# Kernel tuning notes

Measured on AMD Instinct MI355X. Metric: run time of the kernel, lower is better.

The kernel has to match this reference:

```python
import jax, jax.numpy as jnp
import numpy as np

T = 8192          # total prefill tokens (single sequence, cu_seqlens=[0,T])
H = 16            # local num heads (k == v heads)
D = 128           # head_k_dim == head_v_dim
K = 4             # causal conv kernel width
CHUNK = 64        # chunk size used by chunk_kda
EPS = 1e-6


def setup_inputs() -> dict:
    key = jax.random.key(0)
    ks = jax.random.split(key, 6)
    return {
        "mixed_qkv": jax.random.normal(ks[0], (T, 3 * H * D), dtype=jnp.float32),
        "forget_gate": jax.random.normal(ks[1], (T, H * D), dtype=jnp.float32),
        "beta": jax.random.normal(ks[2], (T, H), dtype=jnp.float32),
        "conv_weights": jax.random.normal(ks[3], (3 * H * D, K), dtype=jnp.float32) * 0.1,
        "dt_bias": jax.random.normal(ks[4], (H, D), dtype=jnp.float32),
        "alog": jax.random.normal(ks[5], (H,), dtype=jnp.float32),
    }


def _l2norm(x):
    return x * jax.lax.rsqrt(jnp.sum(x * x, axis=-1, keepdims=True) + EPS)


def _causal_conv1d(x, w):
    # x: [T, C], w: [C, K] depthwise causal conv + SiLU (causal_conv1d_fn)
    xpad = jnp.pad(x, ((K - 1, 0), (0, 0)))
    out = sum(xpad[j:j + T] * w[:, j] for j in range(K))
    return jax.nn.silu(out)


def _kda_forward(mixed_qkv, forget_gate, beta, conv_weights, dt_bias, alog):
    x = _causal_conv1d(mixed_qkv, conv_weights)               # [T, 3*H*D]
    q, k, v = jnp.split(x, [H * D, 2 * H * D], axis=-1)
    q = _l2norm(q.reshape(T, H, D)) * (D ** -0.5)             # scale = head_k_dim^-0.5
    k = _l2norm(k.reshape(T, H, D))
    v = v.reshape(T, H, D)
    # fused_kda_gate: g = -exp(A_log) * softplus(g_raw + dt_bias), per (head, dim)
    g = -jnp.exp(alog)[None, :, None] * jax.nn.softplus(
        forget_gate.reshape(T, H, D) + dt_bias[None])
    decay = jnp.exp(g)                                        # [T, H, D]
    b = jax.nn.sigmoid(beta)                                  # [T, H]

    def step(S, inp):
        # S: [H, Dk, Dv]
        q_t, k_t, v_t, d_t, b_t = inp
        S = S * d_t[:, :, None]                               # per-dim forget gate on key dim
        kmem = jnp.einsum('hk,hkv->hv', k_t, S)
        delta = b_t[:, None] * (v_t - kmem)                   # beta-scaled delta rule
        S = S + jnp.einsum('hk,hv->hkv', k_t, delta)
        o_t = jnp.einsum('hk,hkv->hv', q_t, S)
        return S, o_t

    @jax.checkpoint
    def chunk_fn(S, ch):
        return jax.lax.scan(step, S, ch)

    NC = T // CHUNK
    chunked = lambda a: a.reshape(NC, CHUNK, H, D)
    S0 = jnp.zeros((H, D, D), dtype=jnp.float32)
    _, o = jax.lax.scan(chunk_fn, S0,
                        (chunked(q), chunked(k), chunked(v), chunked(decay),
                         b.reshape(NC, CHUNK, H)))
    return o.reshape(T, H, D)


def reference(mixed_qkv, forget_gate, beta, conv_weights, dt_bias, alog):
    return _kda_forward(mixed_qkv, forget_gate, beta, conv_weights, dt_bias, alog)
```

## Files before the change

### kernel.cpp

```cpp
#include <hip/hip_runtime.h>
#include <math.h>

#define NH 16
#define HD 128
#define CH1 2048
#define CH3 6144
#define CK 64
#define NC 128
#define PCH 132
#define MP 68

#define QT_OFF  0u
#define KBT_OFF 16777216u
#define U0_OFF  33554432u
#define Z_OFF   50331648u
#define W_OFF   67108864u
#define ECG_OFF 75497472u
#define SLAB_OFF 75759616u

__global__ __launch_bounds__(512, 2)
void kda_chunk(const float* __restrict__ mixed, const float* __restrict__ fg,
               const float* __restrict__ beta, const float* __restrict__ cw,
               const float* __restrict__ dtb, const float* __restrict__ alog,
               float* __restrict__ qt_g, float* __restrict__ kbt_g,
               float* __restrict__ u0_g, float* __restrict__ z_g,
               float* __restrict__ w_g, float* __restrict__ ecg_g) {
  __shared__ float lds[35520];
  float* kL  = lds;
  float* qL  = lds + 8448;
  float* cgL = lds + 16896;
  float* ML  = lds + 25344;
  float* NT  = lds + 29696;
  float* GB  = lds + 34048;
  float* bL  = lds + 34816;
  float* nrm = lds + 34880;

  const int tid = threadIdx.x;
  const int bid = blockIdx.x;
  const int c = bid >> 4, h = bid & 15;
  const int t0 = c * CK;
  const float ea = __expf(alog[h]);

  {
    size_t wb = (size_t)bid * 4096;
#pragma unroll
    for (int i = 0; i < 8; ++i) w_g[wb + tid + 512 * i] = 0.f;
  }

  for (int it = 0; it < 16; ++it) {
    int cell = tid + (it << 9);
    int d = cell & 127, t = cell >> 7;
    float x = fg[(size_t)(t0 + t) * CH1 + h * HD + d] + dtb[h * HD + d];
    float sp = (x > 20.f) ? x : log1pf(__expf(x));
    cgL[t * PCH + d] = -ea * sp;
  }
  if (tid < 64) bL[tid] = 1.f / (1.f + __expf(-beta[(size_t)(t0 + tid) * NH + h]));
  __syncthreads();

  if (tid < 128) {
    float a = 0.f;
    for (int t = 0; t < 64; ++t) { a += cgL[t * PCH + tid]; cgL[t * PCH + tid] = a; }
    ecg_g[(size_t)bid * 128 + tid] = __expf(a);
  }

  for (int it = 0; it < 32; ++it) {
    int cell = tid + (it << 9);
    int d = cell & 127, sec = (cell >> 7) & 1, t = cell >> 8;
    int ch = sec * CH1 + h * HD + d;
    float4 w4 = ((const float4*)cw)[ch];
    int rbase = t0 + t - 3;
    float acc;
    if (rbase >= 0) {
      const float* mp = mixed + (size_t)rbase * CH3 + ch;
      acc = mp[0] * w4.x + mp[CH3] * w4.y + mp[2 * CH3] * w4.z + mp[3 * CH3] * w4.w;
    } else {
      acc = 0.f;
      if (rbase + 0 >= 0) acc += mixed[(size_t)(rbase + 0) * CH3 + ch] * w4.x;
      if (rbase + 1 >= 0) acc += mixed[(size_t)(rbase + 1) * CH3 + ch] * w4.y;
      if (rbase + 2 >= 0) acc += mixed[(size_t)(rbase + 2) * CH3 + ch] * w4.z;
      acc += mixed[(size_t)(rbase + 3) * CH3 + ch] * w4.w;
    }
    acc = acc / (1.f + __expf(-acc));
    float* dst = (sec == 0) ? qL : kL;
    dst[t * PCH + d] = acc;
  }
  __syncthreads();

  {
    int sec = tid >> 8, t = (tid >> 2) & 63, r = tid & 3;
    const float* src = (sec == 0) ? qL : kL;
    float s = 0.f;
#pragma unroll
    for (int i = 0; i < 8; ++i) {
      float4 v = *(const float4*)(src + t * PCH + r * 32 + i * 4);
      s += v.x * v.x + v.y * v.y + v.z * v.z + v.w * v.w;
    }
    nrm[tid] = s;
  }
  __syncthreads();
  if (tid < 128) {
    int sec = tid >> 6, t = tid & 63;
    float s = nrm[sec * 256 + t * 4] + nrm[sec * 256 + t * 4 + 1] +
              nrm[sec * 256 + t * 4 + 2] + nrm[sec * 256 + t * 4 + 3];
    float inv = rsqrtf(s + 1e-6f);
    if (sec == 0) inv *= 0.08838834764831845f;
    nrm[512 + tid] = inv;
  }
  __syncthreads();
  for (int it = 0; it < 8; ++it) {
    int f4 = tid + (it << 9);
    int sec = f4 >> 11, t = (f4 >> 5) & 63, d4 = f4 & 31;
    float* dst = (sec == 0) ? qL : kL;
    float inv = nrm[512 + sec * 64 + t];
    float4 v = *(float4*)(dst + t * PCH + d4 * 4);
    v.x *= inv; v.y *= inv; v.z *= inv; v.w *= inv;
    *(float4*)(dst + t * PCH + d4 * 4) = v;
  }
  __syncthreads();

  {
    int tW = tid >> 3, g = tid & 7;
    size_t qb = (size_t)bid * 8192 + g * 1024 + tW * 16;
    size_t kb = (size_t)bid * 8192;
#pragma unroll
    for (int i = 0; i < 4; ++i) {
      int d = g * 16 + 4 * i;
      float4 qv = *(const float4*)(qL + tW * PCH + d);
      float4 cg4 = *(const float4*)(cgL + tW * PCH + d);
      float4 o;
      o.x = qv.x * __expf(cg4.x); o.y = qv.y * __expf(cg4.y);
      o.z = qv.z * __expf(cg4.z); o.w = qv.w * __expf(cg4.w);
      *(float4*)(qt_g + qb + 4 * i) = o;
      float4 kv = *(const float4*)(kL + tW * PCH + d);
      float4 c63 = *(const float4*)(cgL + 63 * PCH + d);
      kbt_g[kb + (size_t)(d + 0) * 64 + tW] = kv.x * __expf(c63.x - cg4.x);
      kbt_g[kb + (size_t)(d + 1) * 64 + tW] = kv.y * __expf(c63.y - cg4.y);
      kbt_g[kb + (size_t)(d + 2) * 64 + tW] = kv.z * __expf(c63.z - cg4.z);
      kbt_g[kb + (size_t)(d + 3) * 64 + tW] = kv.w * __expf(c63.w - cg4.w);
    }
  }

  if (tid < 136) {
    int L = tid;
    int tt = (int)((sqrtf(8.f * L + 1.f) - 1.f) * 0.5f);
    while ((tt + 1) * (tt + 2) / 2 <= L) ++tt;
    while (tt * (tt + 1) / 2 > L) --tt;
    int ss = L - tt * (tt + 1) / 2;
    int ta = tt * 4, sa = ss * 4;
    float accA[16], accW[16];
#pragma unroll
    for (int i = 0; i < 16; ++i) { accA[i] = 0.f; accW[i] = 0.f; }
    for (int d = 0; d < 128; d += 4) {
      float kt[4][4], qt4[4][4], ct[4][4], ks4[4][4], cs4[4][4];
#pragma unroll
      for (int i = 0; i < 4; ++i) {
        *(float4*)kt[i]  = *(const float4*)(kL + (ta + i) * PCH + d);
        *(float4*)qt4[i] = *(const float4*)(qL + (ta + i) * PCH + d);
        *(float4*)ct[i]  = *(const float4*)(cgL + (ta + i) * PCH + d);
        *(float4*)ks4[i] = *(const float4*)(kL + (sa + i) * PCH + d);
        *(float4*)cs4[i] = *(const float4*)(cgL + (sa + i) * PCH + d);
      }
#pragma unroll
      for (int i = 0; i < 4; ++i)
#pragma unroll
        for (int j = 0; j < 4; ++j)
#pragma unroll
          for (int dd = 0; dd < 4; ++dd) {
            float diff = ct[i][dd] - cs4[j][dd];
            float e = __expf(fminf(diff, 0.f));
            float m = e * ks4[j][dd];
            accA[i * 4 + j] += kt[i][dd] * m;
            accW[i * 4 + j] += qt4[i][dd] * m;
          }
    }
    size_t wb = (size_t)bid * 4096;
#pragma unroll
    for (int i = 0; i < 4; ++i)
#pragma unroll
      for (int j = 0; j < 4; ++j) {
        int t = ta + i, s = sa + j;
        if (s < t) ML[t * MP + s] = bL[t] * accA[i * 4 + j];
        float wv = (s <= t) ? accW[i * 4 + j] : 0.f;
        w_g[wb + (size_t)(s >> 3) * 512 + t * 8 + (s & 7)] = wv;
      }
  }
  __syncthreads();

  for (int i = tid; i < 4352; i += 512) NT[i] = 0.f;
  __syncthreads();
  if (tid < 64) {
    int b4 = tid >> 4, j = tid & 15, bo = b4 * 16;
    NT[(bo + j) * MP + bo + j] = 1.f;
    for (int t = j + 1; t < 16; ++t) {
      float s = 0.f;
      for (int sx = j; sx < t; ++sx)
        s += ML[(bo + t) * MP + bo + sx] * NT[(bo + j) * MP + bo + sx];
      NT[(bo + j) * MP + bo + t] = -s;
    }
  }
  __syncthreads();
  for (int lev = 1; lev <= 3; ++lev) {
    int nb = 4 - lev;
    for (int idx = tid; idx < nb * 256; idx += 512) {
      int J = idx >> 8, I = J + lev;
      int i = (idx >> 4) & 15, j = idx & 15;
      float s = 0.f;
      for (int P = J; P < I; ++P)
#pragma unroll 4
        for (int p = 0; p < 16; ++p)
          s += ML[(16 * I + i) * MP + 16 * P + p] * NT[(16 * J + j) * MP + 16 * P + p];
      GB[J * 256 + i * 16 + j] = s;
    }
    __syncthreads();
    for (int idx = tid; idx < nb * 256; idx += 512) {
      int J = idx >> 8, I = J + lev;
      int i = (idx >> 4) & 15, j = idx & 15;
      float s = 0.f;
#pragma unroll 4
      for (int p = 0; p < 16; ++p)
        s += NT[(16 * I + p) * MP + 16 * I + i] * GB[J * 256 + p * 16 + j];
      NT[(16 * J + j) * MP + 16 * I + i] = -s;
    }
    __syncthreads();
  }

  {
    int tW = tid >> 3, g = tid & 7;
    float b = bL[tW];
#pragma unroll
    for (int i = 0; i < 4; ++i) {
      int d = g * 16 + 4 * i;
      float4 kv = *(const float4*)(kL + tW * PCH + d);
      float4 cg4 = *(const float4*)(cgL + tW * PCH + d);
      float4 r;
      r.x = b * kv.x * __expf(cg4.x); r.y = b * kv.y * __expf(cg4.y);
      r.z = b * kv.z * __expf(cg4.z); r.w = b * kv.w * __expf(cg4.w);
      *(float4*)(qL + tW * PCH + d) = r;
    }
  }
  __syncthreads();
  {
    int t4 = tid >> 5, c4 = tid & 31;
    float acc[4][4];
#pragma unroll
    for (int i = 0; i < 4; ++i)
#pragma unroll
      for (int j = 0; j < 4; ++j) acc[i][j] = 0.f;
    for (int s = 0; s < 64; ++s) {
      float nv[4], rv[4];
      *(float4*)nv = *(const float4*)(NT + s * MP + t4 * 4);
      *(float4*)rv = *(const float4*)(qL + s * PCH + c4 * 4);
#pragma unroll
      for (int i = 0; i < 4; ++i)
#pragma unroll
        for (int j = 0; j < 4; ++j) acc[i][j] += nv[i] * rv[j];
    }
    size_t zb = (size_t)bid * 8192 + (size_t)(c4 >> 2) * 1024 + (c4 & 3) * 4;
#pragma unroll
    for (int i = 0; i < 4; ++i) {
      float4 o; o.x = acc[i][0]; o.y = acc[i][1]; o.z = acc[i][2]; o.w = acc[i][3];
      *(float4*)(z_g + zb + (size_t)(t4 * 4 + i) * 16) = o;
    }
  }
  __syncthreads();

  for (int it = 0; it < 16; ++it) {
    int cell = tid + (it << 9);
    int d = cell & 127, t = cell >> 7;
    int ch = 2 * CH1 + h * HD + d;
    float4 w4 = ((const float4*)cw)[ch];
    int rbase = t0 + t - 3;
    float acc;
    if (rbase >= 0) {
      const float* mp = mixed + (size_t)rbase * CH3 + ch;
      acc = mp[0] * w4.x + mp[CH3] * w4.y + mp[2 * CH3] * w4.z + mp[3 * CH3] * w4.w;
    } else {
      acc = 0.f;
      if (rbase + 0 >= 0) acc += mixed[(size_t)(rbase + 0) * CH3 + ch] * w4.x;
      if (rbase + 1 >= 0) acc += mixed[(size_t)(rbase + 1) * CH3 + ch] * w4.y;
      if (rbase + 2 >= 0) acc += mixed[(size_t)(rbase + 2) * CH3 + ch] * w4.z;
      acc += mixed[(size_t)(rbase + 3) * CH3 + ch] * w4.w;
    }
    acc = acc / (1.f + __expf(-acc));
    qL[t * PCH + d] = bL[t] * acc;
  }
  __syncthreads();
  {
    int t4 = tid >> 5, c4 = tid & 31;
    float acc[4][4];
#pragma unroll
    for (int i = 0; i < 4; ++i)
#pragma unroll
      for (int j = 0; j < 4; ++j) acc[i][j] = 0.f;
    for (int s = 0; s < 64; ++s) {
      float nv[4], rv[4];
      *(float4*)nv = *(const float4*)(NT + s * MP + t4 * 4);
      *(float4*)rv = *(const float4*)(qL + s * PCH + c4 * 4);
#pragma unroll
      for (int i = 0; i < 4; ++i)
#pragma unroll
        for (int j = 0; j < 4; ++j) acc[i][j] += nv[i] * rv[j];
    }
#pragma unroll
    for (int i = 0; i < 4; ++i) {
      size_t ob = ((size_t)(t0 + t4 * 4 + i) * NH + h) * HD + c4 * 4;
      float4 o; o.x = acc[i][0]; o.y = acc[i][1]; o.z = acc[i][2]; o.w = acc[i][3];
      *(float4*)(u0_g + ob) = o;
    }
  }
}

__global__ __launch_bounds__(512, 2)
void kda_scan3(const float* __restrict__ qt_g, const float* __restrict__ kbt_g,
               const float* __restrict__ u0_g, const float* __restrict__ z_g,
               const float* __restrict__ w_g, const float* __restrict__ ecg_g,
               float* __restrict__ out, float* __restrict__ slabs) {
  __shared__ float Tp[4224], Op[4224];
  __shared__ float Sl[1024];
  __shared__ float Un[512];
  __shared__ float Ut[512];
  (void)slabs;
  const int tid = threadIdx.x;
  const int bid = blockIdx.x;
  const int h = bid & 15, vg = bid >> 4;
  for (int i = tid; i < 1024; i += 512) Sl[i] = 0.f;
  __syncthreads();
  const int gA = tid >> 6, tA = tid & 63;
  const int tB = tid >> 3, jB = tid & 7;
  const int kC = tid & 127, j2 = tid >> 7;
  for (int c = 0; c < NC; ++c) {
    const int ch = c * 16 + h;
    float z[16], q[16];
    {
      const float* zb = z_g + (size_t)ch * 8192 + gA * 1024 + tA * 16;
      const float* qb = qt_g + (size_t)ch * 8192 + gA * 1024 + tA * 16;
#pragma unroll
      for (int i = 0; i < 4; ++i) {
        *(float4*)(z + 4 * i) = *(const float4*)(zb + 4 * i);
        *(float4*)(q + 4 * i) = *(const float4*)(qb + 4 * i);
      }
    }
    float w8[8];
    {
      const float* wb = w_g + (size_t)ch * 4096 + gA * 512 + tA * 8;
      *(float4*)w8 = *(const float4*)(wb);
      *(float4*)(w8 + 4) = *(const float4*)(wb + 4);
    }
    float kv64[64];
    {
      const float* kb = kbt_g + (size_t)ch * 8192 + (size_t)kC * 64;
#pragma unroll
      for (int t4 = 0; t4 < 16; ++t4)
        *(float4*)(kv64 + 4 * t4) = *(const float4*)(kb + 4 * t4);
    }
    const float u0v = u0_g[((size_t)(c * 64 + tB) * NH + h) * HD + vg * 8 + jB];
    const float eC = ecg_g[(size_t)ch * 128 + kC];

    float Ta[8], Oa[8];
#pragma unroll
    for (int j = 0; j < 8; ++j) { Ta[j] = 0.f; Oa[j] = 0.f; }
    const float* Sg = Sl + gA * 128;
#pragma unroll
    for (int dd = 0; dd < 16; ++dd) {
      float s8[8];
      *(float4*)s8 = *(const float4*)(Sg + dd * 8);
      *(float4*)(s8 + 4) = *(const float4*)(Sg + dd * 8 + 4);
      float zz = z[dd], qq = q[dd];
#pragma unroll
      for (int j = 0; j < 8; ++j) { Ta[j] += zz * s8[j]; Oa[j] += qq * s8[j]; }
    }
#pragma unroll
    for (int j = 0; j < 8; ++j) {
      Tp[gA * 528 + j * 66 + tA] = Ta[j];
      Op[gA * 528 + j * 66 + tA] = Oa[j];
    }
    __syncthreads();

    float Osave;
    {
      float Ts = 0.f, Os = 0.f;
#pragma unroll
      for (int g = 0; g < 8; ++g) {
        Ts += Tp[g * 528 + jB * 66 + tB];
        Os += Op[g * 528 + jB * 66 + tB];
      }
      float U = u0v - Ts;
      Un[tB * 8 + jB] = U;
      Ut[jB * 64 + tB] = U;
      Osave = Os;
    }
    __syncthreads();

    {
      float Wa[8];
#pragma unroll
      for (int j = 0; j < 8; ++j) Wa[j] = 0.f;
#pragma unroll
      for (int sp = 0; sp < 8; ++sp) {
        const float* ur = Un + (gA * 8 + sp) * 8;
        float u8[8];
        *(float4*)u8 = *(const float4*)(ur);
        *(float4*)(u8 + 4) = *(const float4*)(ur + 4);
        float wv = w8[sp];
#pragma unroll
        for (int j = 0; j < 8; ++j) Wa[j] += wv * u8[j];
      }
#pragma unroll
      for (int j = 0; j < 8; ++j) Tp[gA * 528 + j * 66 + tA] = Wa[j];
    }
    __syncthreads();

    {
      float O2 = 0.f;
#pragma unroll
      for (int g = 0; g < 8; ++g) O2 += Tp[g * 528 + jB * 66 + tB];
      out[((size_t)(c * 64 + tB) * NH + h) * HD + vg * 8 + jB] = Osave + O2;
    }

    {
      float a0 = 0.f, a1 = 0.f;
      const float* u0r = Ut + (2 * j2) * 64;
      const float* u1r = Ut + (2 * j2 + 1) * 64;
#pragma unroll
      for (int t4 = 0; t4 < 16; ++t4) {
        float4 ua = *(const float4*)(u0r + 4 * t4);
        float4 ub = *(const float4*)(u1r + 4 * t4);
        a0 += kv64[4 * t4 + 0] * ua.x + kv64[4 * t4 + 1] * ua.y +
              kv64[4 * t4 + 2] * ua.z + kv64[4 * t4 + 3] * ua.w;
        a1 += kv64[4 * t4 + 0] * ub.x + kv64[4 * t4 + 1] * ub.y +
              kv64[4 * t4 + 2] * ub.z + kv64[4 * t4 + 3] * ub.w;
      }
      float* sp2 = Sl + kC * 8 + 2 * j2;
      float s0 = sp2[0], s1 = sp2[1];
      sp2[0] = eC * s0 + a0;
      sp2[1] = eC * s1 + a1;
    }
    __syncthreads();
  }
}

extern "C" void kernel_launch(void* const* d_in, const int* in_sizes, int n_in,
                              void* d_out, int out_size, void* d_ws, size_t ws_size,
                              hipStream_t stream) {
  const float* mixed = (const float*)d_in[0];
  const float* fg    = (const float*)d_in[1];
  const float* beta  = (const float*)d_in[2];
  const float* cw    = (const float*)d_in[3];
  const float* dtb   = (const float*)d_in[4];
  const float* alog  = (const float*)d_in[5];
  float* ws = (float*)d_ws;
  float* qt_g  = ws + QT_OFF;
  float* kbt_g = ws + KBT_OFF;
  float* u0_g  = ws + U0_OFF;
  float* z_g   = ws + Z_OFF;
  float* w_g   = ws + W_OFF;
  float* ecg_g = ws + ECG_OFF;
  float* slabs = ws + SLAB_OFF;

  hipLaunchKernelGGL(kda_chunk, dim3(NC * NH), dim3(512), 0, stream,
                     mixed, fg, beta, cw, dtb, alog,
                     qt_g, kbt_g, u0_g, z_g, w_g, ecg_g);
  hipLaunchKernelGGL(kda_scan3, dim3(256), dim3(512), 0, stream,
                     qt_g, kbt_g, u0_g, z_g, w_g, ecg_g, (float*)d_out, slabs);
  (void)in_sizes; (void)n_in; (void)out_size; (void)ws_size;
}
```

Before: 1.973 ms.

## Double-buffer z/q prefetch across chunks in the scan kernel

Restructures the sequential chunk scan so the z and q loads for the next chunk are issued during the current chunk, using two register buffers and a loop unrolled by two. Empty asm statements force the global loads to complete before the first barrier, which keeps their latency off the serial critical path. The shared-memory padding strides also change (66 to 68, and Ut rows padded to 68). The cost is higher register pressure (an extra 32 floats per thread) under launch bounds of 512 threads and 2 blocks, which may cause spills.

```diff
diff --git a/kernel.cpp b/kernel.cpp
--- a/kernel.cpp
+++ b/kernel.cpp
@@ -310,132 +310,148 @@
   }
 }
 
+#define PT 68
+#define PG 544
+
+#define LOADZQ(zd, qd, cc) do {                                               \
+    const float* zb_ = z_g + (size_t)((cc) * 16 + h) * 8192 + gA * 1024 + tA * 16; \
+    const float* qb_ = qt_g + (size_t)((cc) * 16 + h) * 8192 + gA * 1024 + tA * 16; \
+    _Pragma("unroll")                                                         \
+    for (int i_ = 0; i_ < 4; ++i_) {                                          \
+      *(float4*)((zd) + 4 * i_) = *(const float4*)(zb_ + 4 * i_);             \
+      *(float4*)((qd) + 4 * i_) = *(const float4*)(qb_ + 4 * i_);             \
+    } } while (0)
+
+#define SCAN_BODY(zc, qc, zn, qn, c) do {                                     \
+    const int ch_ = (c) * 16 + h;                                             \
+                          \
+    { const float* kb_ = kbt_g + (size_t)ch_ * 8192 + (size_t)kC * 64;        \
+      _Pragma("unroll")                                                       \
+      for (int t4_ = 0; t4_ < 16; ++t4_)                                      \
+        *(float4*)(kv + 4 * t4_) = *(const float4*)(kb_ + 4 * t4_); }         \
+    { const float* wb_ = w_g + (size_t)ch_ * 4096 + gA * 512 + tA * 8;        \
+      *(float4*)w8 = *(const float4*)wb_;                                     \
+      *(float4*)(w8 + 4) = *(const float4*)(wb_ + 4); }                       \
+    u0v = u0_g[((size_t)((c) * 64 + tB) * NH + h) * HD + vg * 8 + jB];        \
+    eC = ecg_g[(size_t)ch_ * 128 + kC];                                       \
+                  \
+    { const int cn_ = ((c) + 1 < NC) ? (c) + 1 : NC - 1;                      \
+      LOADZQ(zn, qn, cn_); }                                                  \
+              \
+    { float Ta[8], Oa[8];                                                     \
+      _Pragma("unroll")                                                       \
+      for (int j = 0; j < 8; ++j) { Ta[j] = 0.f; Oa[j] = 0.f; }               \
+      const float* Sg = Sl + gA * 128;                                        \
+      _Pragma("unroll")                                                       \
+      for (int dd = 0; dd < 16; ++dd) {                                       \
+        float s8[8];                                                          \
+        *(float4*)s8 = *(const float4*)(Sg + dd * 8);                         \
+        *(float4*)(s8 + 4) = *(const float4*)(Sg + dd * 8 + 4);               \
+        float zz = (zc)[dd], qq = (qc)[dd];                                   \
+        _Pragma("unroll")                                                     \
+        for (int j = 0; j < 8; ++j) { Ta[j] += zz * s8[j]; Oa[j] += qq * s8[j]; } \
+      }                                                                       \
+      _Pragma("unroll")                                                       \
+      for (int j = 0; j < 8; ++j) {                                           \
+        Tp[gA * PG + j * PT + tA] = Ta[j];                                    \
+        Op[gA * PG + j * PT + tA] = Oa[j];                                    \
+      } }                                                                     \
+     \
+     \
+     \
+    _Pragma("unroll")                                                         \
+    for (int i_ = 0; i_ < 64; ++i_) asm volatile("" :: "v"(kv[i_]));          \
+    _Pragma("unroll")                                                         \
+    for (int i_ = 0; i_ < 8; ++i_) asm volatile("" :: "v"(w8[i_]));           \
+    _Pragma("unroll")                                                         \
+    for (int i_ = 0; i_ < 16; ++i_) asm volatile("" :: "v"((zn)[i_]));        \
+    _Pragma("unroll")                                                         \
+    for (int i_ = 0; i_ < 16; ++i_) asm volatile("" :: "v"((qn)[i_]));        \
+    asm volatile("" :: "v"(u0v), "v"(eC));                                    \
+    __syncthreads();                                                          \
+                 \
+    float Osave_;                                                             \
+    { float Ts = 0.f, Os = 0.f;                                               \
+      _Pragma("unroll")                                                       \
+      for (int g = 0; g < 8; ++g) {                                           \
+        Ts += Tp[g * PG + jB * PT + tB];                                      \
+        Os += Op[g * PG + jB * PT + tB];                                      \
+      }                                                                       \
+      float U = u0v - Ts;                                                     \
+      Un[tB * 8 + jB] = U;                                                    \
+      Ut[jB * PT + tB] = U;                                                   \
+      Osave_ = Os; }                                                          \
+    __syncthreads();                                                          \
+                   \
+    { float Wa[8];                                                            \
+      _Pragma("unroll")                                                       \
+      for (int j = 0; j < 8; ++j) Wa[j] = 0.f;                                \
+      _Pragma("unroll")                                                       \
+      for (int sp = 0; sp < 8; ++sp) {                                        \
+        const float* ur = Un + (gA * 8 + sp) * 8;                             \
+        float u8[8];                                                          \
+        *(float4*)u8 = *(const float4*)(ur);                                  \
+        *(float4*)(u8 + 4) = *(const float4*)(ur + 4);                        \
+        float wv = w8[sp];                                                    \
+        _Pragma("unroll")                                                     \
+        for (int j = 0; j < 8; ++j) Wa[j] += wv * u8[j];                      \
+      }                                                                       \
+      _Pragma("unroll")                                                       \
+      for (int j = 0; j < 8; ++j) Tp[gA * PG + j * PT + tA] = Wa[j]; }        \
+    __syncthreads();                                                          \
+                                           \
+    { float O2 = 0.f;                                                         \
+      _Pragma("unroll")                                                       \
+      for (int g = 0; g < 8; ++g) O2 += Tp[g * PG + jB * PT + tB];            \
+      out[((size_t)((c) * 64 + tB) * NH + h) * HD + vg * 8 + jB] = Osave_ + O2; } \
+                                        \
+    { float a0 = 0.f, a1 = 0.f;                                               \
+      const float* u0r = Ut + (2 * j2) * PT;                                  \
+      const float* u1r = Ut + (2 * j2 + 1) * PT;                              \
+      _Pragma("unroll")                                                       \
+      for (int t4 = 0; t4 < 16; ++t4) {                                       \
+        float4 ua = *(const float4*)(u0r + 4 * t4);                           \
+        float4 ub = *(const float4*)(u1r + 4 * t4);                           \
+        a0 += kv[4 * t4 + 0] * ua.x + kv[4 * t4 + 1] * ua.y +                 \
+              kv[4 * t4 + 2] * ua.z + kv[4 * t4 + 3] * ua.w;                  \
+        a1 += kv[4 * t4 + 0] * ub.x + kv[4 * t4 + 1] * ub.y +                 \
+              kv[4 * t4 + 2] * ub.z + kv[4 * t4 + 3] * ub.w;                  \
+      }                                                                       \
+      float* sp2 = Sl + kC * 8 + 2 * j2;                                      \
+      float s0 = sp2[0], s1 = sp2[1];                                         \
+      sp2[0] = eC * s0 + a0;                                                  \
+      sp2[1] = eC * s1 + a1; }                                                \
+    __syncthreads();                                                          \
+  } while (0)
+
 __global__ __launch_bounds__(512, 2)
 void kda_scan3(const float* __restrict__ qt_g, const float* __restrict__ kbt_g,
                const float* __restrict__ u0_g, const float* __restrict__ z_g,
                const float* __restrict__ w_g, const float* __restrict__ ecg_g,
                float* __restrict__ out, float* __restrict__ slabs) {
-  __shared__ float Tp[4224], Op[4224];
+  __shared__ float Tp[4352], Op[4352];
   __shared__ float Sl[1024];
   __shared__ float Un[512];
-  __shared__ float Ut[512];
+  __shared__ float Ut[544];
   (void)slabs;
   const int tid = threadIdx.x;
   const int bid = blockIdx.x;
   const int h = bid & 15, vg = bid >> 4;
-  for (int i = tid; i < 1024; i += 512) Sl[i] = 0.f;
-  __syncthreads();
   const int gA = tid >> 6, tA = tid & 63;
   const int tB = tid >> 3, jB = tid & 7;
   const int kC = tid & 127, j2 = tid >> 7;
-  for (int c = 0; c < NC; ++c) {
-    const int ch = c * 16 + h;
-    float z[16], q[16];
-    {
-      const float* zb = z_g + (size_t)ch * 8192 + gA * 1024 + tA * 16;
-      const float* qb = qt_g + (size_t)ch * 8192 + gA * 1024 + tA * 16;
-#pragma unroll
-      for (int i = 0; i < 4; ++i) {
-        *(float4*)(z + 4 * i) = *(const float4*)(zb + 4 * i);
-        *(float4*)(q + 4 * i) = *(const float4*)(qb + 4 * i);
-      }
-    }
-    float w8[8];
-    {
-      const float* wb = w_g + (size_t)ch * 4096 + gA * 512 + tA * 8;
-      *(float4*)w8 = *(const float4*)(wb);
-      *(float4*)(w8 + 4) = *(const float4*)(wb + 4);
-    }
-    float kv64[64];
-    {
-      const float* kb = kbt_g + (size_t)ch * 8192 + (size_t)kC * 64;
-#pragma unroll
-      for (int t4 = 0; t4 < 16; ++t4)
-        *(float4*)(kv64 + 4 * t4) = *(const float4*)(kb + 4 * t4);
-    }
-    const float u0v = u0_g[((size_t)(c * 64 + tB) * NH + h) * HD + vg * 8 + jB];
-    const float eC = ecg_g[(size_t)ch * 128 + kC];
-
-    float Ta[8], Oa[8];
-#pragma unroll
-    for (int j = 0; j < 8; ++j) { Ta[j] = 0.f; Oa[j] = 0.f; }
-    const float* Sg = Sl + gA * 128;
-#pragma unroll
-    for (int dd = 0; dd < 16; ++dd) {
-      float s8[8];
-      *(float4*)s8 = *(const float4*)(Sg + dd * 8);
-      *(float4*)(s8 + 4) = *(const float4*)(Sg + dd * 8 + 4);
-      float zz = z[dd], qq = q[dd];
-#pragma unroll
-      for (int j = 0; j < 8; ++j) { Ta[j] += zz * s8[j]; Oa[j] += qq * s8[j]; }
-    }
-#pragma unroll
-    for (int j = 0; j < 8; ++j) {
-      Tp[gA * 528 + j * 66 + tA] = Ta[j];
-      Op[gA * 528 + j * 66 + tA] = Oa[j];
-    }
-    __syncthreads();
-
-    float Osave;
-    {
-      float Ts = 0.f, Os = 0.f;
-#pragma unroll
-      for (int g = 0; g < 8; ++g) {
-        Ts += Tp[g * 528 + jB * 66 + tB];
-        Os += Op[g * 528 + jB * 66 + tB];
-      }
-      float U = u0v - Ts;
-      Un[tB * 8 + jB] = U;
-      Ut[jB * 64 + tB] = U;
-      Osave = Os;
-    }
-    __syncthreads();
-
-    {
-      float Wa[8];
-#pragma unroll
-      for (int j = 0; j < 8; ++j) Wa[j] = 0.f;
-#pragma unroll
-      for (int sp = 0; sp < 8; ++sp) {
-        const float* ur = Un + (gA * 8 + sp) * 8;
-        float u8[8];
-        *(float4*)u8 = *(const float4*)(ur);
-        *(float4*)(u8 + 4) = *(const float4*)(ur + 4);
-        float wv = w8[sp];
-#pragma unroll
-        for (int j = 0; j < 8; ++j) Wa[j] += wv * u8[j];
-      }
-#pragma unroll
-      for (int j = 0; j < 8; ++j) Tp[gA * 528 + j * 66 + tA] = Wa[j];
-    }
-    __syncthreads();
-
-    {
-      float O2 = 0.f;
-#pragma unroll
-      for (int g = 0; g < 8; ++g) O2 += Tp[g * 528 + jB * 66 + tB];
-      out[((size_t)(c * 64 + tB) * NH + h) * HD + vg * 8 + jB] = Osave + O2;
-    }
-
-    {
-      float a0 = 0.f, a1 = 0.f;
-      const float* u0r = Ut + (2 * j2) * 64;
-      const float* u1r = Ut + (2 * j2 + 1) * 64;
-#pragma unroll
-      for (int t4 = 0; t4 < 16; ++t4) {
-        float4 ua = *(const float4*)(u0r + 4 * t4);
-        float4 ub = *(const float4*)(u1r + 4 * t4);
-        a0 += kv64[4 * t4 + 0] * ua.x + kv64[4 * t4 + 1] * ua.y +
-              kv64[4 * t4 + 2] * ua.z + kv64[4 * t4 + 3] * ua.w;
-        a1 += kv64[4 * t4 + 0] * ub.x + kv64[4 * t4 + 1] * ub.y +
-              kv64[4 * t4 + 2] * ub.z + kv64[4 * t4 + 3] * ub.w;
-      }
-      float* sp2 = Sl + kC * 8 + 2 * j2;
-      float s0 = sp2[0], s1 = sp2[1];
-      sp2[0] = eC * s0 + a0;
-      sp2[1] = eC * s1 + a1;
-    }
-    __syncthreads();
+
+  float zA[16], qA[16], zB[16], qB[16];
+  float kv[64], w8[8];
+  float u0v, eC;
+
+  LOADZQ(zA, qA, 0);
+  for (int i = tid; i < 1024; i += 512) Sl[i] = 0.f;
+  __syncthreads();
+
+  for (int c = 0; c < NC; c += 2) {
+    SCAN_BODY(zA, qA, zB, qB, c);
+    SCAN_BODY(zB, qB, zA, qA, c + 1);
   }
 }
 
```

Result: slower. 2.161 ms (+9.5%).

## Split scan across 4-wide value slices and specialize thread roles per phase

Applied to the files above, without the earlier changes.

The sequential chunk scan now partitions the value dimension into 32 groups of 4 columns instead of 16 groups of 8, doubling the grid to 512 blocks so more CUs run the latency-bound recurrence in parallel. Within a block, the lower half of threads handles the U reduction and the state update while the upper half handles the output reduction and store, with padded shared-memory strides. Each block still reloads full z, q, w and kbt tiles for every chunk, so redundant global traffic doubles. Launch bounds also rise to 4 blocks per CU.

```diff
diff --git a/kernel.cpp b/kernel.cpp
--- a/kernel.cpp
+++ b/kernel.cpp
@@ -310,24 +310,29 @@
   }
 }
 
-__global__ __launch_bounds__(512, 2)
+#define PT 68
+#define PG 272
+
+__global__ __launch_bounds__(512, 4)
 void kda_scan3(const float* __restrict__ qt_g, const float* __restrict__ kbt_g,
                const float* __restrict__ u0_g, const float* __restrict__ z_g,
                const float* __restrict__ w_g, const float* __restrict__ ecg_g,
                float* __restrict__ out, float* __restrict__ slabs) {
-  __shared__ float Tp[4224], Op[4224];
-  __shared__ float Sl[1024];
-  __shared__ float Un[512];
-  __shared__ float Ut[512];
+  __shared__ float Tp[2176], Op[2176];
+  __shared__ float Sl[512];
+  __shared__ float Un[256];
+  __shared__ float Ut[272];
   (void)slabs;
   const int tid = threadIdx.x;
   const int bid = blockIdx.x;
   const int h = bid & 15, vg = bid >> 4;
-  for (int i = tid; i < 1024; i += 512) Sl[i] = 0.f;
-  __syncthreads();
   const int gA = tid >> 6, tA = tid & 63;
-  const int tB = tid >> 3, jB = tid & 7;
-  const int kC = tid & 127, j2 = tid >> 7;
+  const int tB = (tid >> 2) & 63, jB = tid & 3;
+  const int kC = tid & 127, j2 = (tid >> 7) & 1;
+
+  for (int i = tid; i < 512; i += 512) Sl[i] = 0.f;
+  __syncthreads();
+
   for (int c = 0; c < NC; ++c) {
     const int ch = c * 16 + h;
     float z[16], q[16];
@@ -346,91 +351,88 @@
       *(float4*)w8 = *(const float4*)(wb);
       *(float4*)(w8 + 4) = *(const float4*)(wb + 4);
     }
-    float kv64[64];
+    const float u0v = u0_g[((size_t)(c * 64 + tB) * NH + h) * HD + vg * 4 + jB];
+    float kv[64], eC = 0.f;
+    if (tid < 256) {
+      const float* kb = kbt_g + (size_t)ch * 8192 + (size_t)kC * 64;
+#pragma unroll
+      for (int t4 = 0; t4 < 16; ++t4)
+        *(float4*)(kv + 4 * t4) = *(const float4*)(kb + 4 * t4);
+      eC = ecg_g[(size_t)ch * 128 + kC];
+    }
+
     {
-      const float* kb = kbt_g + (size_t)ch * 8192 + (size_t)kC * 64;
-#pragma unroll
-      for (int t4 = 0; t4 < 16; ++t4)
-        *(float4*)(kv64 + 4 * t4) = *(const float4*)(kb + 4 * t4);
-    }
-    const float u0v = u0_g[((size_t)(c * 64 + tB) * NH + h) * HD + vg * 8 + jB];
-    const float eC = ecg_g[(size_t)ch * 128 + kC];
-
-    float Ta[8], Oa[8];
-#pragma unroll
-    for (int j = 0; j < 8; ++j) { Ta[j] = 0.f; Oa[j] = 0.f; }
-    const float* Sg = Sl + gA * 128;
-#pragma unroll
-    for (int dd = 0; dd < 16; ++dd) {
-      float s8[8];
-      *(float4*)s8 = *(const float4*)(Sg + dd * 8);
-      *(float4*)(s8 + 4) = *(const float4*)(Sg + dd * 8 + 4);
-      float zz = z[dd], qq = q[dd];
-#pragma unroll
-      for (int j = 0; j < 8; ++j) { Ta[j] += zz * s8[j]; Oa[j] += qq * s8[j]; }
-    }
-#pragma unroll
-    for (int j = 0; j < 8; ++j) {
-      Tp[gA * 528 + j * 66 + tA] = Ta[j];
-      Op[gA * 528 + j * 66 + tA] = Oa[j];
-    }
-    __syncthreads();
-
-    float Osave;
+      float Ta[4], Oa[4];
+#pragma unroll
+      for (int j = 0; j < 4; ++j) { Ta[j] = 0.f; Oa[j] = 0.f; }
+#pragma unroll
+      for (int dd = 0; dd < 16; ++dd) {
+        float s4[4];
+        *(float4*)s4 = *(const float4*)(Sl + (gA * 16 + dd) * 4);
+        float zz = z[dd], qq = q[dd];
+#pragma unroll
+        for (int j = 0; j < 4; ++j) { Ta[j] += zz * s4[j]; Oa[j] += qq * s4[j]; }
+      }
+#pragma unroll
+      for (int j = 0; j < 4; ++j) {
+        Tp[gA * PG + j * PT + tA] = Ta[j];
+        Op[gA * PG + j * PT + tA] = Oa[j];
+      }
+    }
+    __syncthreads();
+
+    float Osave = 0.f;
+    if (tid < 256) {
+      float Ts = 0.f;
+#pragma unroll
+      for (int g = 0; g < 8; ++g) Ts += Tp[g * PG + jB * PT + tB];
+      float U = u0v - Ts;
+      Un[tB * 4 + jB] = U;
+      Ut[jB * PT + tB] = U;
+    } else {
+      float Os = 0.f;
+#pragma unroll
+      for (int g = 0; g < 8; ++g) Os += Op[g * PG + jB * PT + tB];
+      Osave = Os;
+    }
+    __syncthreads();
+
     {
-      float Ts = 0.f, Os = 0.f;
-#pragma unroll
-      for (int g = 0; g < 8; ++g) {
-        Ts += Tp[g * 528 + jB * 66 + tB];
-        Os += Op[g * 528 + jB * 66 + tB];
-      }
-      float U = u0v - Ts;
-      Un[tB * 8 + jB] = U;
-      Ut[jB * 64 + tB] = U;
-      Osave = Os;
-    }
-    __syncthreads();
-
-    {
-      float Wa[8];
-#pragma unroll
-      for (int j = 0; j < 8; ++j) Wa[j] = 0.f;
+      float Wa[4];
+#pragma unroll
+      for (int j = 0; j < 4; ++j) Wa[j] = 0.f;
 #pragma unroll
       for (int sp = 0; sp < 8; ++sp) {
-        const float* ur = Un + (gA * 8 + sp) * 8;
-        float u8[8];
-        *(float4*)u8 = *(const float4*)(ur);
-        *(float4*)(u8 + 4) = *(const float4*)(ur + 4);
+        float u4[4];
+        *(float4*)u4 = *(const float4*)(Un + (gA * 8 + sp) * 4);
         float wv = w8[sp];
 #pragma unroll
-        for (int j = 0; j < 8; ++j) Wa[j] += wv * u8[j];
-      }
-#pragma unroll
-      for (int j = 0; j < 8; ++j) Tp[gA * 528 + j * 66 + tA] = Wa[j];
-    }
-    __syncthreads();
-
-    {
+        for (int j = 0; j < 4; ++j) Wa[j] += wv * u4[j];
+      }
+#pragma unroll
+      for (int j = 0; j < 4; ++j) Tp[gA * PG + j * PT + tA] = Wa[j];
+    }
+    __syncthreads();
+
+    if (tid >= 256) {
       float O2 = 0.f;
 #pragma unroll
-      for (int g = 0; g < 8; ++g) O2 += Tp[g * 528 + jB * 66 + tB];
-      out[((size_t)(c * 64 + tB) * NH + h) * HD + vg * 8 + jB] = Osave + O2;
-    }
-
-    {
+      for (int g = 0; g < 8; ++g) O2 += Tp[g * PG + jB * PT + tB];
+      out[((size_t)(c * 64 + tB) * NH + h) * HD + vg * 4 + jB] = Osave + O2;
+    } else {
       float a0 = 0.f, a1 = 0.f;
-      const float* u0r = Ut + (2 * j2) * 64;
-      const float* u1r = Ut + (2 * j2 + 1) * 64;
+      const float* u0r = Ut + (2 * j2) * PT;
+      const float* u1r = Ut + (2 * j2 + 1) * PT;
 #pragma unroll
       for (int t4 = 0; t4 < 16; ++t4) {
         float4 ua = *(const float4*)(u0r + 4 * t4);
         float4 ub = *(const float4*)(u1r + 4 * t4);
-        a0 += kv64[4 * t4 + 0] * ua.x + kv64[4 * t4 + 1] * ua.y +
-              kv64[4 * t4 + 2] * ua.z + kv64[4 * t4 + 3] * ua.w;
-        a1 += kv64[4 * t4 + 0] * ub.x + kv64[4 * t4 + 1] * ub.y +
-              kv64[4 * t4 + 2] * ub.z + kv64[4 * t4 + 3] * ub.w;
-      }
-      float* sp2 = Sl + kC * 8 + 2 * j2;
+        a0 += kv[4 * t4 + 0] * ua.x + kv[4 * t4 + 1] * ua.y +
+              kv[4 * t4 + 2] * ua.z + kv[4 * t4 + 3] * ua.w;
+        a1 += kv[4 * t4 + 0] * ub.x + kv[4 * t4 + 1] * ub.y +
+              kv[4 * t4 + 2] * ub.z + kv[4 * t4 + 3] * ub.w;
+      }
+      float* sp2 = Sl + kC * 4 + 2 * j2;
       float s0 = sp2[0], s1 = sp2[1];
       sp2[0] = eC * s0 + a0;
       sp2[1] = eC * s1 + a1;
@@ -460,7 +462,7 @@
   hipLaunchKernelGGL(kda_chunk, dim3(NC * NH), dim3(512), 0, stream,
                      mixed, fg, beta, cw, dtb, alog,
                      qt_g, kbt_g, u0_g, z_g, w_g, ecg_g);
-  hipLaunchKernelGGL(kda_scan3, dim3(256), dim3(512), 0, stream,
+  hipLaunchKernelGGL(kda_scan3, dim3(512), dim3(512), 0, stream,
                      qt_g, kbt_g, u0_g, z_g, w_g, ecg_g, (float*)d_out, slabs);
   (void)in_sizes; (void)n_in; (void)out_size; (void)ws_size;
 }
```

Result: slower. 2.264 ms (+14.7%).

## Warp-specialize scan into state-update and output groups, split chunk-prep dot over D

Applied to the files above, without the earlier changes.

The sequential scan kernel now splits its 512 threads into two halves. One half computes U and the state update, the other computes the output correction and writes the previous chunk's output, which removes one block barrier per chunk and defers the output write to the next iteration. Shared-memory strides are padded to cut bank conflicts. In the chunk-prep kernel, the triangular 4x4-tile dot products are split across two threads over halves of the head dimension and combined through shared memory, doubling active threads. The cost is an extra barrier and partial-sum traffic in prep, plus higher register and shared-memory use in the scan.

```diff
diff --git a/kernel.cpp b/kernel.cpp
--- a/kernel.cpp
+++ b/kernel.cpp
@@ -140,25 +140,27 @@
     }
   }
 
-  if (tid < 136) {
-    int L = tid;
+  int taD = 0, saD = 0;
+  float accA[16], accW[16];
+  if (tid < 272) {
+    int L = tid >> 1, dh = tid & 1;
     int tt = (int)((sqrtf(8.f * L + 1.f) - 1.f) * 0.5f);
     while ((tt + 1) * (tt + 2) / 2 <= L) ++tt;
     while (tt * (tt + 1) / 2 > L) --tt;
     int ss = L - tt * (tt + 1) / 2;
-    int ta = tt * 4, sa = ss * 4;
-    float accA[16], accW[16];
+    taD = tt * 4; saD = ss * 4;
 #pragma unroll
     for (int i = 0; i < 16; ++i) { accA[i] = 0.f; accW[i] = 0.f; }
-    for (int d = 0; d < 128; d += 4) {
+    int d0 = dh << 6;
+    for (int d = d0; d < d0 + 64; d += 4) {
       float kt[4][4], qt4[4][4], ct[4][4], ks4[4][4], cs4[4][4];
 #pragma unroll
       for (int i = 0; i < 4; ++i) {
-        *(float4*)kt[i]  = *(const float4*)(kL + (ta + i) * PCH + d);
-        *(float4*)qt4[i] = *(const float4*)(qL + (ta + i) * PCH + d);
-        *(float4*)ct[i]  = *(const float4*)(cgL + (ta + i) * PCH + d);
-        *(float4*)ks4[i] = *(const float4*)(kL + (sa + i) * PCH + d);
-        *(float4*)cs4[i] = *(const float4*)(cgL + (sa + i) * PCH + d);
+        *(float4*)kt[i]  = *(const float4*)(kL + (taD + i) * PCH + d);
+        *(float4*)qt4[i] = *(const float4*)(qL + (taD + i) * PCH + d);
+        *(float4*)ct[i]  = *(const float4*)(cgL + (taD + i) * PCH + d);
+        *(float4*)ks4[i] = *(const float4*)(kL + (saD + i) * PCH + d);
+        *(float4*)cs4[i] = *(const float4*)(cgL + (saD + i) * PCH + d);
       }
 #pragma unroll
       for (int i = 0; i < 4; ++i)
@@ -173,12 +175,28 @@
             accW[i * 4 + j] += qt4[i][dd] * m;
           }
     }
+    if (dh) {
+#pragma unroll
+      for (int i = 0; i < 16; ++i) {
+        NT[L * 32 + i] = accA[i];
+        NT[L * 32 + 16 + i] = accW[i];
+      }
+    }
+  }
+  __syncthreads();
+  if (tid < 272 && !(tid & 1)) {
+    int L = tid >> 1;
+#pragma unroll
+    for (int i = 0; i < 16; ++i) {
+      accA[i] += NT[L * 32 + i];
+      accW[i] += NT[L * 32 + 16 + i];
+    }
     size_t wb = (size_t)bid * 4096;
 #pragma unroll
     for (int i = 0; i < 4; ++i)
 #pragma unroll
       for (int j = 0; j < 4; ++j) {
-        int t = ta + i, s = sa + j;
+        int t = taD + i, s = saD + j;
         if (s < t) ML[t * MP + s] = bL[t] * accA[i * 4 + j];
         float wv = (s <= t) ? accW[i * 4 + j] : 0.f;
         w_g[wb + (size_t)(s >> 3) * 512 + t * 8 + (s & 7)] = wv;
@@ -310,24 +328,35 @@
   }
 }
 
+#define PT 68
+#define PG 544
+
 __global__ __launch_bounds__(512, 2)
 void kda_scan3(const float* __restrict__ qt_g, const float* __restrict__ kbt_g,
                const float* __restrict__ u0_g, const float* __restrict__ z_g,
                const float* __restrict__ w_g, const float* __restrict__ ecg_g,
                float* __restrict__ out, float* __restrict__ slabs) {
-  __shared__ float Tp[4224], Op[4224];
-  __shared__ float Sl[1024];
+  __shared__ float Tp[4352], Op[4352];
+  __shared__ float Wp[2176];
+  __shared__ float Sl[1536];
   __shared__ float Un[512];
-  __shared__ float Ut[512];
+  __shared__ float Ut[544];
   (void)slabs;
   const int tid = threadIdx.x;
   const int bid = blockIdx.x;
   const int h = bid & 15, vg = bid >> 4;
-  for (int i = tid; i < 1024; i += 512) Sl[i] = 0.f;
-  __syncthreads();
   const int gA = tid >> 6, tA = tid & 63;
-  const int tB = tid >> 3, jB = tid & 7;
-  const int kC = tid & 127, j2 = tid >> 7;
+  const int tH = (tid & 255) >> 2;
+  const int jH = (tid & 3) << 1;
+  const int kC = tid & 127;
+  const int jq = ((tid >> 7) & 1) << 2;
+  const int gB = (tid >> 6) & 3;
+
+  for (int i = tid; i < 1536; i += 512) Sl[i] = 0.f;
+  __syncthreads();
+
+  float OsA = 0.f, OsB = 0.f;
+
   for (int c = 0; c < NC; ++c) {
     const int ch = c * 16 + h;
     float z[16], q[16];
@@ -340,102 +369,130 @@
         *(float4*)(q + 4 * i) = *(const float4*)(qb + 4 * i);
       }
     }
-    float w8[8];
+    float w16[16];
+    float u0a = 0.f, u0b = 0.f;
+    float kv[64], eC = 0.f;
+    if (tid < 256) {
+      const float* kb = kbt_g + (size_t)ch * 8192 + (size_t)kC * 64;
+#pragma unroll
+      for (int t4 = 0; t4 < 16; ++t4)
+        *(float4*)(kv + 4 * t4) = *(const float4*)(kb + 4 * t4);
+      eC = ecg_g[(size_t)ch * 128 + kC];
+      const float* ub = u0_g + ((size_t)(c * 64 + tH) * NH + h) * HD + vg * 8 + jH;
+      u0a = ub[0]; u0b = ub[1];
+    } else {
+      const float* wb = w_g + (size_t)ch * 4096 + (size_t)(gB * 2) * 512 + tA * 8;
+      *(float4*)w16       = *(const float4*)(wb);
+      *(float4*)(w16 + 4) = *(const float4*)(wb + 4);
+      *(float4*)(w16 + 8)  = *(const float4*)(wb + 512);
+      *(float4*)(w16 + 12) = *(const float4*)(wb + 516);
+    }
+
+    if (tid >= 256 && c > 0) {
+      float O2a = 0.f, O2b = 0.f;
+#pragma unroll
+      for (int g = 0; g < 4; ++g) {
+        O2a += Wp[g * PG + jH * PT + tH];
+        O2b += Wp[g * PG + (jH + 1) * PT + tH];
+      }
+      float* ob = out + ((size_t)((c - 1) * 64 + tH) * NH + h) * HD + vg * 8 + jH;
+      ob[0] = OsA + O2a; ob[1] = OsB + O2b;
+    }
     {
-      const float* wb = w_g + (size_t)ch * 4096 + gA * 512 + tA * 8;
-      *(float4*)w8 = *(const float4*)(wb);
-      *(float4*)(w8 + 4) = *(const float4*)(wb + 4);
-    }
-    float kv64[64];
-    {
-      const float* kb = kbt_g + (size_t)ch * 8192 + (size_t)kC * 64;
-#pragma unroll
-      for (int t4 = 0; t4 < 16; ++t4)
-        *(float4*)(kv64 + 4 * t4) = *(const float4*)(kb + 4 * t4);
-    }
-    const float u0v = u0_g[((size_t)(c * 64 + tB) * NH + h) * HD + vg * 8 + jB];
-    const float eC = ecg_g[(size_t)ch * 128 + kC];
-
-    float Ta[8], Oa[8];
-#pragma unroll
-    for (int j = 0; j < 8; ++j) { Ta[j] = 0.f; Oa[j] = 0.f; }
-    const float* Sg = Sl + gA * 128;
-#pragma unroll
-    for (int dd = 0; dd < 16; ++dd) {
-      float s8[8];
-      *(float4*)s8 = *(const float4*)(Sg + dd * 8);
-      *(float4*)(s8 + 4) = *(const float4*)(Sg + dd * 8 + 4);
-      float zz = z[dd], qq = q[dd];
-#pragma unroll
-      for (int j = 0; j < 8; ++j) { Ta[j] += zz * s8[j]; Oa[j] += qq * s8[j]; }
-    }
-#pragma unroll
-    for (int j = 0; j < 8; ++j) {
-      Tp[gA * 528 + j * 66 + tA] = Ta[j];
-      Op[gA * 528 + j * 66 + tA] = Oa[j];
+      float Ta[8], Oa[8];
+#pragma unroll
+      for (int j = 0; j < 8; ++j) { Ta[j] = 0.f; Oa[j] = 0.f; }
+#pragma unroll
+      for (int dd = 0; dd < 16; ++dd) {
+        float s8[8];
+        const float* sr = Sl + (gA * 16 + dd) * 12;
+        *(float4*)s8 = *(const float4*)(sr);
+        *(float4*)(s8 + 4) = *(const float4*)(sr + 4);
+        float zz = z[dd], qq = q[dd];
+#pragma unroll
+        for (int j = 0; j < 8; ++j) { Ta[j] += zz * s8[j]; Oa[j] += qq * s8[j]; }
+      }
+#pragma unroll
+      for (int j = 0; j < 8; ++j) {
+        Tp[gA * PG + j * PT + tA] = Ta[j];
+        Op[gA * PG + j * PT + tA] = Oa[j];
+      }
     }
     __syncthreads();
 
-    float Osave;
-    {
-      float Ts = 0.f, Os = 0.f;
+    if (tid < 256) {
+      float Tsa = 0.f, Tsb = 0.f;
 #pragma unroll
       for (int g = 0; g < 8; ++g) {
-        Ts += Tp[g * 528 + jB * 66 + tB];
-        Os += Op[g * 528 + jB * 66 + tB];
-      }
-      float U = u0v - Ts;
-      Un[tB * 8 + jB] = U;
-      Ut[jB * 64 + tB] = U;
-      Osave = Os;
+        Tsa += Tp[g * PG + jH * PT + tH];
+        Tsb += Tp[g * PG + (jH + 1) * PT + tH];
+      }
+      float Ua = u0a - Tsa, Ub = u0b - Tsb;
+      Un[tH * 8 + jH] = Ua; Un[tH * 8 + jH + 1] = Ub;
+      Ut[jH * PT + tH] = Ua; Ut[(jH + 1) * PT + tH] = Ub;
+    } else {
+      float Os1 = 0.f, Os2 = 0.f;
+#pragma unroll
+      for (int g = 0; g < 8; ++g) {
+        Os1 += Op[g * PG + jH * PT + tH];
+        Os2 += Op[g * PG + (jH + 1) * PT + tH];
+      }
+      OsA = Os1; OsB = Os2;
     }
     __syncthreads();
 
-    {
+    if (tid < 256) {
+      float a0 = 0.f, a1 = 0.f, a2 = 0.f, a3 = 0.f;
+      const float* u0r = Ut + (jq + 0) * PT;
+      const float* u1r = Ut + (jq + 1) * PT;
+      const float* u2r = Ut + (jq + 2) * PT;
+      const float* u3r = Ut + (jq + 3) * PT;
+#pragma unroll
+      for (int t4 = 0; t4 < 16; ++t4) {
+        float k0 = kv[4 * t4], k1 = kv[4 * t4 + 1], k2 = kv[4 * t4 + 2], k3 = kv[4 * t4 + 3];
+        float4 ua = *(const float4*)(u0r + 4 * t4);
+        float4 ub = *(const float4*)(u1r + 4 * t4);
+        float4 uc = *(const float4*)(u2r + 4 * t4);
+        float4 ud = *(const float4*)(u3r + 4 * t4);
+        a0 += k0 * ua.x + k1 * ua.y + k2 * ua.z + k3 * ua.w;
+        a1 += k0 * ub.x + k1 * ub.y + k2 * ub.z + k3 * ub.w;
+        a2 += k0 * uc.x + k1 * uc.y + k2 * uc.z + k3 * uc.w;
+        a3 += k0 * ud.x + k1 * ud.y + k2 * ud.z + k3 * ud.w;
+      }
+      float* sp = Sl + kC * 12 + jq;
+      float4 s = *(float4*)sp;
+      s.x = eC * s.x + a0; s.y = eC * s.y + a1;
+      s.z = eC * s.z + a2; s.w = eC * s.w + a3;
+      *(float4*)sp = s;
+    } else {
       float Wa[8];
 #pragma unroll
       for (int j = 0; j < 8; ++j) Wa[j] = 0.f;
 #pragma unroll
-      for (int sp = 0; sp < 8; ++sp) {
-        const float* ur = Un + (gA * 8 + sp) * 8;
+      for (int sp = 0; sp < 16; ++sp) {
+        const float* ur = Un + (gB * 16 + sp) * 8;
         float u8[8];
         *(float4*)u8 = *(const float4*)(ur);
         *(float4*)(u8 + 4) = *(const float4*)(ur + 4);
-        float wv = w8[sp];
+        float wv = w16[sp];
 #pragma unroll
         for (int j = 0; j < 8; ++j) Wa[j] += wv * u8[j];
       }
 #pragma unroll
-      for (int j = 0; j < 8; ++j) Tp[gA * 528 + j * 66 + tA] = Wa[j];
+      for (int j = 0; j < 8; ++j) Wp[gB * PG + j * PT + tA] = Wa[j];
     }
     __syncthreads();
-
-    {
-      float O2 = 0.f;
-#pragma unroll
-      for (int g = 0; g < 8; ++g) O2 += Tp[g * 528 + jB * 66 + tB];
-      out[((size_t)(c * 64 + tB) * NH + h) * HD + vg * 8 + jB] = Osave + O2;
-    }
-
-    {
-      float a0 = 0.f, a1 = 0.f;
-      const float* u0r = Ut + (2 * j2) * 64;
-      const float* u1r = Ut + (2 * j2 + 1) * 64;
-#pragma unroll
-      for (int t4 = 0; t4 < 16; ++t4) {
-        float4 ua = *(const float4*)(u0r + 4 * t4);
-        float4 ub = *(const float4*)(u1r + 4 * t4);
-        a0 += kv64[4 * t4 + 0] * ua.x + kv64[4 * t4 + 1] * ua.y +
-              kv64[4 * t4 + 2] * ua.z + kv64[4 * t4 + 3] * ua.w;
-        a1 += kv64[4 * t4 + 0] * ub.x + kv64[4 * t4 + 1] * ub.y +
-              kv64[4 * t4 + 2] * ub.z + kv64[4 * t4 + 3] * ub.w;
-      }
-      float* sp2 = Sl + kC * 8 + 2 * j2;
-      float s0 = sp2[0], s1 = sp2[1];
-      sp2[0] = eC * s0 + a0;
-      sp2[1] = eC * s1 + a1;
-    }
-    __syncthreads();
+  }
+
+  if (tid >= 256) {
+    float O2a = 0.f, O2b = 0.f;
+#pragma unroll
+    for (int g = 0; g < 4; ++g) {
+      O2a += Wp[g * PG + jH * PT + tH];
+      O2b += Wp[g * PG + (jH + 1) * PT + tH];
+    }
+    float* ob = out + ((size_t)((NC - 1) * 64 + tH) * NH + h) * HD + vg * 8 + jH;
+    ob[0] = OsA + O2a; ob[1] = OsB + O2b;
   }
 }
 
```

Measured after the change: 1.847 ms. 1.07x faster.
